# Kernel tuning notes

Hardware: AMD Instinct MI355X
Metric: run time of the kernel (lower is better)

Reference implementation:

```python
import jax, jax.numpy as jnp
import numpy as np

EPS_BN = 1e-5
CLAMP_MAX = 1e-10  # nn.Hardtanh(min_val=0, max_val=1e-10) on squared dists


def _three_nn(xyz1, xyz2):
    # xyz1: (b, n, 3), xyz2: (b, m, 3) -> sq dists (b, n, 3), idx (b, n, 3)
    d2 = (jnp.sum(xyz1 ** 2, -1, keepdims=True)
          - 2.0 * jnp.einsum('bnc,bmc->bnm', xyz1, xyz2)
          + jnp.sum(xyz2 ** 2, -1)[:, None, :])  # (b, n, m)
    neg, idx = jax.lax.top_k(-d2, 3)
    return -neg, idx


def _conv_bn_relu(x, W, b, g, beta):
    # x: (b, n, cin); 1x1 Conv2d == pointwise linear, BN over (batch, spatial)
    y = jnp.einsum('bnc,oc->bno', x, W) + b
    mean = jnp.mean(y, axis=(0, 1))
    var = jnp.mean((y - mean) ** 2, axis=(0, 1))
    y = (y - mean) * jax.lax.rsqrt(var + EPS_BN) * g + beta
    return jax.nn.relu(y)


def setup_inputs() -> dict:
    key = jax.random.key(0)
    ks = jax.random.split(key, 8)
    b, n, m, c1, c2 = 16, 4096, 1024, 256, 512
    mlp, dimin = [256, 256], [c1 + c2, 256]
    inp = {
        'xyz1': jax.random.normal(ks[0], (b, n, 3), jnp.float32),
        'xyz2': jax.random.normal(ks[1], (b, m, 3), jnp.float32),
        'points1': jax.random.normal(ks[2], (b, n, c1), jnp.float32),
        'points2': jax.random.normal(ks[3], (b, m, c2), jnp.float32),
        'W1': jax.random.normal(ks[4], (mlp[0], dimin[0]), jnp.float32) * 0.02,
        'b1': jnp.zeros((mlp[0],), jnp.float32),
        'g1': jnp.ones((mlp[0],), jnp.float32),
        'beta1': jnp.zeros((mlp[0],), jnp.float32),
        'W2': jax.random.normal(ks[5], (mlp[1], dimin[1]), jnp.float32) * 0.02,
        'b2': jnp.zeros((mlp[1],), jnp.float32),
        'g2': jnp.ones((mlp[1],), jnp.float32),
        'beta2': jnp.zeros((mlp[1],), jnp.float32),
    }
    return inp


def reference(xyz1, xyz2, points1, points2, W1, b1, g1, beta1, W2, b2, g2, beta2):
    dist, idx = _three_nn(xyz1, xyz2)                     # (b, n, 3)
    dist = jnp.clip(dist, 0.0, CLAMP_MAX)                 # Hardtanh(0, 1e-10)
    inv = 1.0 / dist
    weight = inv / jnp.sum(inv, axis=2, keepdims=True)    # (b, n, 3)
    neigh = jax.vmap(lambda p, i: p[i])(points2, idx)     # (b, n, 3, c2)
    interp = jnp.einsum('bnk,bnkc->bnc', weight, neigh)   # (b, n, c2)
    feat = jnp.concatenate([interp, points1], axis=2)     # (b, n, c2+c1)
    feat = _conv_bn_relu(feat, W1, b1, g1, beta1)
    feat = _conv_bn_relu(feat, W2, b2, g2, beta2)
    return jnp.transpose(feat, (0, 2, 1))                 # (b, c_out, n)
```

## Files before the change

### kernel.cpp

```cpp
#include <hip/hip_runtime.h>

typedef unsigned short u16;
typedef short sh8 __attribute__((ext_vector_type(8)));
typedef float floatx4 __attribute__((ext_vector_type(4)));
typedef float float4v __attribute__((ext_vector_type(4)));
typedef u16 us8 __attribute__((ext_vector_type(8)));

#define NB    16
#define NPTS  4096
#define MPTS  1024
#define CC1   256
#define CC2   512
#define KK1   768
#define CCO   256
#define MT    (NB*NPTS)
#define MZ    (NB*MPTS)

__device__ __forceinline__ float b2f(u16 u) {
    union { unsigned i; float f; } v; v.i = ((unsigned)u) << 16; return v.f;
}
__device__ __forceinline__ u16 f2b(float f) {
    union { float f; unsigned i; } v; v.f = f;
    unsigned u = v.i;
    unsigned r = (u + 0x7fffu + ((u >> 16) & 1u)) >> 16;
    return (u16)r;
}
__device__ __forceinline__ float ldv(const void* p, size_t i, int f32) {
    return f32 ? ((const float*)p)[i] : b2f(((const u16*)p)[i]);
}
__device__ __forceinline__ void stv(void* p, size_t i, int f32, float v) {
    if (f32) ((float*)p)[i] = v; else ((u16*)p)[i] = f2b(v);
}
__device__ __forceinline__ void gl_lds16(const void* g, void* l) {
    __builtin_amdgcn_global_load_lds(
        (const __attribute__((address_space(1))) void*)g,
        (__attribute__((address_space(3))) void*)l, 16, 0, 0);
}

__global__ void Pointnet_fp_module_33071248179394_kernel(
        const unsigned* g1bits, int* flag, float* stats) {
    int i = blockIdx.x * 256 + threadIdx.x;
    stats[i] = 0.f;
    if (i == 0) flag[0] = (g1bits[0] == 0x3F800000u) ? 1 : 0;
}

__global__ __launch_bounds__(256) void three_nn_k(
        const int* flagp, const void* xyz1, const void* xyz2,
        int* nidx, float* nw) {
    __shared__ float4 P[MPTS];
    __shared__ float md[256][3];
    __shared__ int   mi[256][3];
    const int f32 = flagp[0];
    const int bi = blockIdx.x >> 6;
    const int chunk = blockIdx.x & 63;
    const int t = threadIdx.x;
    const int ql = t & 63, sp = t >> 6;

    for (int p = t; p < MPTS; p += 256) {
        size_t s = (size_t)(bi * MPTS + p) * 3;
        P[p] = make_float4(ldv(xyz2, s, f32), ldv(xyz2, s + 1, f32),
                           ldv(xyz2, s + 2, f32), 0.f);
    }
    __syncthreads();

    const int q = chunk * 64 + ql;
    size_t s1 = (size_t)(bi * NPTS + q) * 3;
    const float qx = ldv(xyz1, s1 + 0, f32);
    const float qy = ldv(xyz1, s1 + 1, f32);
    const float qz = ldv(xyz1, s1 + 2, f32);

    float d0 = 3e38f, d1 = 3e38f, dv2 = 3e38f;
    int i0 = -1, i1 = -1, i2 = -1;
    const int jbeg = sp * 256, jend = jbeg + 256;
    #pragma unroll 4
    for (int j = jbeg; j < jend; j++) {
        float4 p = P[j];
        float dx = qx - p.x;
        float dy = qy - p.y;
        float dz = qz - p.z;
        float dd = fmaf(dx, dx, fmaf(dy, dy, dz * dz));
        if (dd < dv2) {
            if (dd < d0)      { dv2 = d1; i2 = i1; d1 = d0; i1 = i0; d0 = dd; i0 = j; }
            else if (dd < d1) { dv2 = d1; i2 = i1; d1 = dd; i1 = j; }
            else              { dv2 = dd; i2 = j; }
        }
    }
    md[t][0] = d0;  md[t][1] = d1;  md[t][2] = dv2;
    mi[t][0] = i0;  mi[t][1] = i1;  mi[t][2] = i2;
    __syncthreads();

    if (t < 64) {
        float b0 = 3e38f, b1 = 3e38f, b2v = 3e38f;
        int j0 = -1, j1 = -1, j2 = -1;
        #pragma unroll
        for (int s = 0; s < 4; s++) {
            int base = s * 64 + t;
            #pragma unroll
            for (int k = 0; k < 3; k++) {
                float d = md[base][k];
                int ji = mi[base][k];
                if (d < b0)      { b2v = b1; j2 = j1; b1 = b0; j1 = j0; b0 = d; j0 = ji; }
                else if (d < b1) { b2v = b1; j2 = j1; b1 = d; j1 = ji; }
                else if (d < b2v){ b2v = d; j2 = ji; }
            }
        }
        float e0 = fminf(fmaxf(b0, 0.f), 1e-10f);
        float e1 = fminf(fmaxf(b1, 0.f), 1e-10f);
        float e2 = fminf(fmaxf(b2v, 0.f), 1e-10f);
        float v0 = 1.0f / e0, v1 = 1.0f / e1, v2 = 1.0f / e2;
        float s = v0 + v1 + v2;
        const size_t gq = ((size_t)bi * NPTS + chunk * 64 + t) * 3;
        nidx[gq + 0] = j0; nidx[gq + 1] = j1; nidx[gq + 2] = j2;
        nw[gq + 0] = v0 / s; nw[gq + 1] = v1 / s; nw[gq + 2] = v2 / s;
    }
}

__global__ __launch_bounds__(256) void cvt_vec_k(
        const int* flagp, const void* src, u16* dst) {
    const int f32 = flagp[0];
    const size_t i = ((size_t)blockIdx.x * 256 + threadIdx.x) * 8;
    us8 o;
    if (f32) {
        float4v a = *(const float4v*)((const float*)src + i);
        float4v b = *(const float4v*)((const float*)src + i + 4);
        #pragma unroll
        for (int k = 0; k < 4; k++) { o[k] = f2b(a[k]); o[k + 4] = f2b(b[k]); }
    } else {
        o = *(const us8*)((const u16*)src + i);
    }
    *(us8*)(dst + i) = o;
}

__global__ __launch_bounds__(256) void cvt_slice_k(
        const int* flagp, const void* src, u16* dst,
        int stride, int off, int cshift) {
    const int f32 = flagp[0];
    const int i = blockIdx.x * 256 + threadIdx.x;
    const int r = i >> cshift, c = i & ((1 << cshift) - 1);
    dst[i] = f2b(ldv(src, (size_t)r * stride + off + c, f32));
}

template<int K>
__global__ __launch_bounds__(256, 2) void gemm_bt(
        const int* flagp, const u16* __restrict__ A, const u16* __restrict__ B,
        const void* __restrict__ bias, u16* __restrict__ Y) {
    __shared__ u16 As[128 * 32];
    __shared__ u16 Bs[128 * 32];
    const int f32 = flagp[0];
    const int tid = threadIdx.x;
    const int m0 = blockIdx.x * 128;
    const int n0 = blockIdx.y * 128;
    const int wave = tid >> 6, lane = tid & 63;
    const int wm = wave & 1, wn = wave >> 1;
    const int l16 = lane & 15, quad = lane >> 4;

    floatx4 acc[4][4];
    #pragma unroll
    for (int i = 0; i < 4; i++)
        #pragma unroll
        for (int j = 0; j < 4; j++)
            acc[i][j] = (floatx4){0.f, 0.f, 0.f, 0.f};

    for (int kb = 0; kb < K; kb += 32) {
        __syncthreads();
        #pragma unroll
        for (int tt = 0; tt < 2; tt++) {
            int chunk = tid + tt * 256;
            int row = chunk >> 2, c4 = chunk & 3;
            gl_lds16(A + (size_t)(m0 + row) * K + kb + c4 * 8, As + chunk * 8);
            gl_lds16(B + (size_t)(n0 + row) * K + kb + c4 * 8, Bs + chunk * 8);
        }
        __syncthreads();

        sh8 af[4], bfr[4];
        #pragma unroll
        for (int i = 0; i < 4; i++)
            af[i] = *(const sh8*)(As + (wm * 64 + i * 16 + l16) * 32 + quad * 8);
        #pragma unroll
        for (int j = 0; j < 4; j++)
            bfr[j] = *(const sh8*)(Bs + (wn * 64 + j * 16 + l16) * 32 + quad * 8);
        #pragma unroll
        for (int i = 0; i < 4; i++)
            #pragma unroll
            for (int j = 0; j < 4; j++)
                acc[i][j] = __builtin_amdgcn_mfma_f32_16x16x32_bf16(
                                af[i], bfr[j], acc[i][j], 0, 0, 0);
    }

    #pragma unroll
    for (int i = 0; i < 4; i++) {
        #pragma unroll
        for (int j = 0; j < 4; j++) {
            int col = n0 + wn * 64 + j * 16 + l16;
            float bv = ldv(bias, col, f32);
            #pragma unroll
            for (int r = 0; r < 4; r++) {
                int row = m0 + wm * 64 + i * 16 + quad * 4 + r;
                Y[(size_t)row * CCO + col] = f2b(acc[i][j][r] + bv);
            }
        }
    }
}

__global__ __launch_bounds__(256, 2) void gemm_p_k(
        const int* flagp, const u16* __restrict__ A, const u16* __restrict__ B,
        const void* __restrict__ bias, const int* __restrict__ nidx,
        const float* __restrict__ nw, const u16* __restrict__ Z,
        u16* __restrict__ Y) {
    __shared__ u16 As[128 * 32];
    __shared__ u16 Bs[128 * 32];
    __shared__ int   sIdx[128 * 3];
    __shared__ float sW[128 * 3];
    const int f32 = flagp[0];
    const int tid = threadIdx.x;
    const int m0 = blockIdx.x * 128;
    const int n0 = blockIdx.y * 128;
    const int wave = tid >> 6, lane = tid & 63;
    const int wm = wave & 1, wn = wave >> 1;
    const int l16 = lane & 15, quad = lane >> 4;
    const int zbase = (m0 >> 12) << 10;

    if (tid < 128) {
        size_t q3 = (size_t)(m0 + tid) * 3;
        #pragma unroll
        for (int k = 0; k < 3; k++) {
            sIdx[tid * 3 + k] = nidx[q3 + k];
            sW[tid * 3 + k]   = nw[q3 + k];
        }
    }

    floatx4 acc[4][4];
    #pragma unroll
    for (int i = 0; i < 4; i++)
        #pragma unroll
        for (int j = 0; j < 4; j++)
            acc[i][j] = (floatx4){0.f, 0.f, 0.f, 0.f};

    constexpr int K = 256;
    for (int kb = 0; kb < K; kb += 32) {
        __syncthreads();
        #pragma unroll
        for (int tt = 0; tt < 2; tt++) {
            int chunk = tid + tt * 256;
            int row = chunk >> 2, c4 = chunk & 3;
            gl_lds16(A + (size_t)(m0 + row) * K + kb + c4 * 8, As + chunk * 8);
            gl_lds16(B + (size_t)(n0 + row) * K + kb + c4 * 8, Bs + chunk * 8);
        }
        __syncthreads();

        sh8 af[4], bfr[4];
        #pragma unroll
        for (int i = 0; i < 4; i++)
            af[i] = *(const sh8*)(As + (wm * 64 + i * 16 + l16) * 32 + quad * 8);
        #pragma unroll
        for (int j = 0; j < 4; j++)
            bfr[j] = *(const sh8*)(Bs + (wn * 64 + j * 16 + l16) * 32 + quad * 8);
        #pragma unroll
        for (int i = 0; i < 4; i++)
            #pragma unroll
            for (int j = 0; j < 4; j++)
                acc[i][j] = __builtin_amdgcn_mfma_f32_16x16x32_bf16(
                                af[i], bfr[j], acc[i][j], 0, 0, 0);
    }

    #pragma unroll
    for (int i = 0; i < 4; i++) {
        #pragma unroll
        for (int r = 0; r < 4; r++) {
            int rl = wm * 64 + i * 16 + quad * 4 + r;
            int i0 = sIdx[rl * 3 + 0], i1 = sIdx[rl * 3 + 1], i2 = sIdx[rl * 3 + 2];
            float w0 = sW[rl * 3 + 0], w1 = sW[rl * 3 + 1], w2 = sW[rl * 3 + 2];
            const u16* z0 = Z + (size_t)(zbase + i0) * CCO;
            const u16* z1 = Z + (size_t)(zbase + i1) * CCO;
            const u16* z2 = Z + (size_t)(zbase + i2) * CCO;
            #pragma unroll
            for (int j = 0; j < 4; j++) {
                int col = n0 + wn * 64 + j * 16 + l16;
                float v = acc[i][j][r] + ldv(bias, col, f32)
                        + w0 * b2f(z0[col]) + w1 * b2f(z1[col]) + w2 * b2f(z2[col]);
                Y[(size_t)(m0 + rl) * CCO + col] = f2b(v);
            }
        }
    }
}

__global__ void bn_stats_k(const u16* Y, float* sum, float* sq) {
    const int c = threadIdx.x;
    const int r0 = blockIdx.x * 128;
    float s = 0.f, ss = 0.f;
    for (int r = 0; r < 128; r++) {
        float v = b2f(Y[(size_t)(r0 + r) * CCO + c]);
        s += v; ss += v * v;
    }
    atomicAdd(&sum[c], s);
    atomicAdd(&sq[c], ss);
}

__global__ void bn_apply_k(const int* flagp, u16* Y,
                           const float* sum, const float* sq,
                           const void* g, const void* beta) {
    const int f32 = flagp[0];
    const int idx = blockIdx.x * 256 + threadIdx.x;
    const int c = idx & (CCO - 1);
    const float invM = 1.0f / (float)MT;
    float mean = sum[c] * invM;
    float var = sq[c] * invM - mean * mean;
    float sc = rsqrtf(var + 1e-5f) * ldv(g, c, f32);
    float sh = ldv(beta, c, f32) - mean * sc;
    float v = b2f(Y[idx]) * sc + sh;
    Y[idx] = f2b(fmaxf(v, 0.f));
}

__global__ void bn_out_k(const int* flagp, const u16* Y, void* Out,
                         const float* sum, const float* sq,
                         const void* g, const void* beta) {
    __shared__ float tile[64][65];
    const int f32 = flagp[0];
    const int bi = blockIdx.z;
    const int p0 = blockIdx.x * 64;
    const int c0 = blockIdx.y * 64;
    const int t = threadIdx.x;
    const int cr = t & 63, rq = t >> 6;
    const float invM = 1.0f / (float)MT;

    const int c = c0 + cr;
    float mean = sum[c] * invM;
    float var = sq[c] * invM - mean * mean;
    float sc = rsqrtf(var + 1e-5f) * ldv(g, c, f32);
    float sh = ldv(beta, c, f32) - mean * sc;

    for (int r = rq; r < 64; r += 4) {
        int m = bi * NPTS + p0 + r;
        float v = b2f(Y[(size_t)m * CCO + c]) * sc + sh;
        tile[r][cr] = fmaxf(v, 0.f);
    }
    __syncthreads();
    for (int r = rq; r < 64; r += 4) {
        size_t o = ((size_t)bi * CCO + (c0 + r)) * NPTS + p0 + cr;
        stv(Out, o, f32, tile[cr][r]);
    }
}

extern "C" void kernel_launch(void* const* d_in, const int* in_sizes, int n_in,
                              void* d_out, int out_size, void* d_ws, size_t ws_size,
                              hipStream_t stream) {
    const void* xyz1    = d_in[0];
    const void* xyz2    = d_in[1];
    const void* points1 = d_in[2];
    const void* points2 = d_in[3];
    const void* W1      = d_in[4];
    const void* b1      = d_in[5];
    const void* g1      = d_in[6];
    const void* be1     = d_in[7];
    const void* W2      = d_in[8];
    const void* b2      = d_in[9];
    const void* g2      = d_in[10];
    const void* be2     = d_in[11];
    char* ws = (char*)d_ws;

    int*   flag  = (int*)(ws + 0);
    float* sum1  = (float*)(ws + 4096);
    float* sq1   = (float*)(ws + 5120);
    float* sum2  = (float*)(ws + 6144);
    float* sq2   = (float*)(ws + 7168);
    float* zeros = (float*)(ws + 8192);
    int*   nidx  = (int*)(ws + 20480);
    float* nw    = (float*)(ws + 806912);
    u16* Wa   = (u16*)(ws + 2097152);
    u16* Wbp  = (u16*)(ws + 2359296);
    u16* W2b  = (u16*)(ws + 2490368);
    u16* Z    = (u16*)(ws + 2621440);
    u16* p2b  = (u16*)(ws + 11010048ULL);
    u16* p1b  = (u16*)(ws + 27787264ULL);
    u16* y1   = (u16*)(ws + 61341696ULL);
    u16* y2   = (u16*)(ws + 94896128ULL);

    Pointnet_fp_module_33071248179394_kernel<<<dim3(16), dim3(256), 0, stream>>>(
        (const unsigned*)g1, flag, (float*)(ws + 4096));
    cvt_slice_k<<<dim3(CCO * CC2 / 256), dim3(256), 0, stream>>>(flag, W1, Wa, KK1, 0, 9);
    cvt_slice_k<<<dim3(CCO * CC1 / 256), dim3(256), 0, stream>>>(flag, W1, Wbp, KK1, CC2, 8);
    cvt_slice_k<<<dim3(CCO * CCO / 256), dim3(256), 0, stream>>>(flag, W2, W2b, CCO, 0, 8);
    cvt_vec_k<<<dim3(MZ * CC2 / 2048), dim3(256), 0, stream>>>(flag, points2, p2b);
    cvt_vec_k<<<dim3(MT * CC1 / 2048), dim3(256), 0, stream>>>(flag, points1, p1b);
    three_nn_k<<<dim3(1024), dim3(256), 0, stream>>>(flag, xyz1, xyz2, nidx, nw);
    gemm_bt<CC2><<<dim3(MZ / 128, CCO / 128), dim3(256), 0, stream>>>(flag, p2b, Wa, zeros, Z);
    gemm_p_k<<<dim3(MT / 128, CCO / 128), dim3(256), 0, stream>>>(
        flag, p1b, Wbp, b1, nidx, nw, Z, y1);
    bn_stats_k<<<dim3(512), dim3(256), 0, stream>>>(y1, sum1, sq1);
    bn_apply_k<<<dim3(MT), dim3(256), 0, stream>>>(flag, y1, sum1, sq1, g1, be1);
    gemm_bt<CCO><<<dim3(MT / 128, CCO / 128), dim3(256), 0, stream>>>(flag, y1, W2b, b2, y2);
    bn_stats_k<<<dim3(512), dim3(256), 0, stream>>>(y2, sum2, sq2);
    bn_out_k<<<dim3(64, 4, NB), dim3(256), 0, stream>>>(flag, y2, d_out, sum2, sq2, g2, be2);
}
```

Baseline: 359.3 us.

## Fuse BN statistics into GEMM epilogues and merge conversion kernels

```diff
diff --git a/kernel.cpp b/kernel.cpp
--- a/kernel.cpp
+++ b/kernel.cpp
@@ -44,19 +44,19 @@
     if (i == 0) flag[0] = (g1bits[0] == 0x3F800000u) ? 1 : 0;
 }
 
-__global__ __launch_bounds__(256) void three_nn_k(
+__global__ __launch_bounds__(512) void three_nn_k(
         const int* flagp, const void* xyz1, const void* xyz2,
         int* nidx, float* nw) {
     __shared__ float4 P[MPTS];
-    __shared__ float md[256][3];
-    __shared__ int   mi[256][3];
+    __shared__ float md[512][3];
+    __shared__ int   mi[512][3];
     const int f32 = flagp[0];
     const int bi = blockIdx.x >> 6;
     const int chunk = blockIdx.x & 63;
     const int t = threadIdx.x;
     const int ql = t & 63, sp = t >> 6;
 
-    for (int p = t; p < MPTS; p += 256) {
+    for (int p = t; p < MPTS; p += 512) {
         size_t s = (size_t)(bi * MPTS + p) * 3;
         P[p] = make_float4(ldv(xyz2, s, f32), ldv(xyz2, s + 1, f32),
                            ldv(xyz2, s + 2, f32), 0.f);
@@ -71,7 +71,7 @@
 
     float d0 = 3e38f, d1 = 3e38f, dv2 = 3e38f;
     int i0 = -1, i1 = -1, i2 = -1;
-    const int jbeg = sp * 256, jend = jbeg + 256;
+    const int jbeg = sp * 128, jend = jbeg + 128;
     #pragma unroll 4
     for (int j = jbeg; j < jend; j++) {
         float4 p = P[j];
@@ -93,7 +93,7 @@
         float b0 = 3e38f, b1 = 3e38f, b2v = 3e38f;
         int j0 = -1, j1 = -1, j2 = -1;
         #pragma unroll
-        for (int s = 0; s < 4; s++) {
+        for (int s = 0; s < 8; s++) {
             int base = s * 64 + t;
             #pragma unroll
             for (int k = 0; k < 3; k++) {
@@ -115,37 +115,53 @@
     }
 }
 
-__global__ __launch_bounds__(256) void cvt_vec_k(
-        const int* flagp, const void* src, u16* dst) {
-    const int f32 = flagp[0];
-    const size_t i = ((size_t)blockIdx.x * 256 + threadIdx.x) * 8;
+__global__ __launch_bounds__(256) void cvt_w_k(
+        const int* flagp, const void* W1, const void* W2,
+        u16* Wa, u16* Wbp, u16* W2b) {
+    const int f32 = flagp[0];
+    const int i = blockIdx.x * 256 + threadIdx.x;
+    if (i < CCO * CC2) {
+        int r = i >> 9, c = i & 511;
+        Wa[i] = f2b(ldv(W1, (size_t)r * KK1 + c, f32));
+    } else if (i < CCO * CC2 + CCO * CC1) {
+        int k = i - CCO * CC2;
+        int r = k >> 8, c = k & 255;
+        Wbp[k] = f2b(ldv(W1, (size_t)r * KK1 + CC2 + c, f32));
+    } else {
+        int k = i - CCO * CC2 - CCO * CC1;
+        W2b[k] = f2b(ldv(W2, k, f32));
+    }
+}
+
+__global__ __launch_bounds__(256) void cvt_pts_k(
+        const int* flagp, const void* p2, const void* p1,
+        u16* p2b, u16* p1b) {
+    const int f32 = flagp[0];
+    size_t i = ((size_t)blockIdx.x * 256 + threadIdx.x) * 8;
+    const size_t N2 = (size_t)MZ * CC2;
+    const void* src; u16* dst; size_t off;
+    if (i < N2) { src = p2; dst = p2b; off = i; }
+    else        { src = p1; dst = p1b; off = i - N2; }
     us8 o;
     if (f32) {
-        float4v a = *(const float4v*)((const float*)src + i);
-        float4v b = *(const float4v*)((const float*)src + i + 4);
+        float4v a = *(const float4v*)((const float*)src + off);
+        float4v b = *(const float4v*)((const float*)src + off + 4);
         #pragma unroll
         for (int k = 0; k < 4; k++) { o[k] = f2b(a[k]); o[k + 4] = f2b(b[k]); }
     } else {
-        o = *(const us8*)((const u16*)src + i);
-    }
-    *(us8*)(dst + i) = o;
-}
-
-__global__ __launch_bounds__(256) void cvt_slice_k(
-        const int* flagp, const void* src, u16* dst,
-        int stride, int off, int cshift) {
-    const int f32 = flagp[0];
-    const int i = blockIdx.x * 256 + threadIdx.x;
-    const int r = i >> cshift, c = i & ((1 << cshift) - 1);
-    dst[i] = f2b(ldv(src, (size_t)r * stride + off + c, f32));
-}
-
-template<int K>
+        o = *(const us8*)((const u16*)src + off);
+    }
+    *(us8*)(dst + off) = o;
+}
+
+template<int K, bool STATS>
 __global__ __launch_bounds__(256, 2) void gemm_bt(
         const int* flagp, const u16* __restrict__ A, const u16* __restrict__ B,
-        const void* __restrict__ bias, u16* __restrict__ Y) {
+        const void* __restrict__ bias, u16* __restrict__ Y,
+        float* __restrict__ sum, float* __restrict__ sq) {
     __shared__ u16 As[128 * 32];
     __shared__ u16 Bs[128 * 32];
+    __shared__ float sSum[128], sSq[128];
     const int f32 = flagp[0];
     const int tid = threadIdx.x;
     const int m0 = blockIdx.x * 128;
@@ -154,6 +170,8 @@
     const int wm = wave & 1, wn = wave >> 1;
     const int l16 = lane & 15, quad = lane >> 4;
 
+    if (STATS && tid < 128) { sSum[tid] = 0.f; sSq[tid] = 0.f; }
+
     floatx4 acc[4][4];
     #pragma unroll
     for (int i = 0; i < 4; i++)
@@ -187,6 +205,7 @@
                                 af[i], bfr[j], acc[i][j], 0, 0, 0);
     }
 
+    float cs[4] = {0.f, 0.f, 0.f, 0.f}, css[4] = {0.f, 0.f, 0.f, 0.f};
     #pragma unroll
     for (int i = 0; i < 4; i++) {
         #pragma unroll
@@ -196,8 +215,23 @@
             #pragma unroll
             for (int r = 0; r < 4; r++) {
                 int row = m0 + wm * 64 + i * 16 + quad * 4 + r;
-                Y[(size_t)row * CCO + col] = f2b(acc[i][j][r] + bv);
+                float v = acc[i][j][r] + bv;
+                if (STATS) { cs[j] += v; css[j] += v * v; }
+                Y[(size_t)row * CCO + col] = f2b(v);
             }
+        }
+    }
+    if (STATS) {
+        #pragma unroll
+        for (int j = 0; j < 4; j++) {
+            int cl = wn * 64 + j * 16 + l16;
+            atomicAdd(&sSum[cl], cs[j]);
+            atomicAdd(&sSq[cl], css[j]);
+        }
+        __syncthreads();
+        if (tid < 128) {
+            atomicAdd(&sum[n0 + tid], sSum[tid]);
+            atomicAdd(&sq[n0 + tid], sSq[tid]);
         }
     }
 }
@@ -206,11 +240,12 @@
         const int* flagp, const u16* __restrict__ A, const u16* __restrict__ B,
         const void* __restrict__ bias, const int* __restrict__ nidx,
         const float* __restrict__ nw, const u16* __restrict__ Z,
-        u16* __restrict__ Y) {
+        u16* __restrict__ Y, float* __restrict__ sum, float* __restrict__ sq) {
     __shared__ u16 As[128 * 32];
     __shared__ u16 Bs[128 * 32];
     __shared__ int   sIdx[128 * 3];
     __shared__ float sW[128 * 3];
+    __shared__ float sSum[128], sSq[128];
     const int f32 = flagp[0];
     const int tid = threadIdx.x;
     const int m0 = blockIdx.x * 128;
@@ -227,6 +262,7 @@
             sIdx[tid * 3 + k] = nidx[q3 + k];
             sW[tid * 3 + k]   = nw[q3 + k];
         }
+        sSum[tid] = 0.f; sSq[tid] = 0.f;
     }
 
     floatx4 acc[4][4];
@@ -263,6 +299,7 @@
                                 af[i], bfr[j], acc[i][j], 0, 0, 0);
     }
 
+    float cs[4] = {0.f, 0.f, 0.f, 0.f}, css[4] = {0.f, 0.f, 0.f, 0.f};
     #pragma unroll
     for (int i = 0; i < 4; i++) {
         #pragma unroll
@@ -278,37 +315,51 @@
                 int col = n0 + wn * 64 + j * 16 + l16;
                 float v = acc[i][j][r] + ldv(bias, col, f32)
                         + w0 * b2f(z0[col]) + w1 * b2f(z1[col]) + w2 * b2f(z2[col]);
+                cs[j] += v; css[j] += v * v;
                 Y[(size_t)(m0 + rl) * CCO + col] = f2b(v);
             }
         }
     }
-}
-
-__global__ void bn_stats_k(const u16* Y, float* sum, float* sq) {
-    const int c = threadIdx.x;
-    const int r0 = blockIdx.x * 128;
-    float s = 0.f, ss = 0.f;
-    for (int r = 0; r < 128; r++) {
-        float v = b2f(Y[(size_t)(r0 + r) * CCO + c]);
-        s += v; ss += v * v;
-    }
-    atomicAdd(&sum[c], s);
-    atomicAdd(&sq[c], ss);
-}
-
-__global__ void bn_apply_k(const int* flagp, u16* Y,
-                           const float* sum, const float* sq,
-                           const void* g, const void* beta) {
-    const int f32 = flagp[0];
-    const int idx = blockIdx.x * 256 + threadIdx.x;
-    const int c = idx & (CCO - 1);
-    const float invM = 1.0f / (float)MT;
-    float mean = sum[c] * invM;
-    float var = sq[c] * invM - mean * mean;
-    float sc = rsqrtf(var + 1e-5f) * ldv(g, c, f32);
-    float sh = ldv(beta, c, f32) - mean * sc;
-    float v = b2f(Y[idx]) * sc + sh;
-    Y[idx] = f2b(fmaxf(v, 0.f));
+    #pragma unroll
+    for (int j = 0; j < 4; j++) {
+        int cl = wn * 64 + j * 16 + l16;
+        atomicAdd(&sSum[cl], cs[j]);
+        atomicAdd(&sSq[cl], css[j]);
+    }
+    __syncthreads();
+    if (tid < 128) {
+        atomicAdd(&sum[n0 + tid], sSum[tid]);
+        atomicAdd(&sq[n0 + tid], sSq[tid]);
+    }
+}
+
+__global__ __launch_bounds__(256) void bn_apply_k(
+        const int* flagp, u16* Y, const float* sum, const float* sq,
+        const void* g, const void* beta) {
+    __shared__ float ssc[CCO], ssh[CCO];
+    const int f32 = flagp[0];
+    const int t = threadIdx.x;
+    {
+        const float invM = 1.0f / (float)MT;
+        float mean = sum[t] * invM;
+        float var = sq[t] * invM - mean * mean;
+        float sc = rsqrtf(var + 1e-5f) * ldv(g, t, f32);
+        ssc[t] = sc;
+        ssh[t] = ldv(beta, t, f32) - mean * sc;
+    }
+    __syncthreads();
+    const size_t base = ((size_t)blockIdx.x * 256 + t) * 16;
+    const int c0 = (int)(base & (CCO - 1));
+    us8 a = *(const us8*)(Y + base);
+    us8 b = *(const us8*)(Y + base + 8);
+    us8 oa, ob;
+    #pragma unroll
+    for (int k = 0; k < 8; k++) {
+        oa[k] = f2b(fmaxf(b2f((u16)a[k]) * ssc[c0 + k] + ssh[c0 + k], 0.f));
+        ob[k] = f2b(fmaxf(b2f((u16)b[k]) * ssc[c0 + 8 + k] + ssh[c0 + 8 + k], 0.f));
+    }
+    *(us8*)(Y + base) = oa;
+    *(us8*)(Y + base + 8) = ob;
 }
 
 __global__ void bn_out_k(const int* flagp, const u16* Y, void* Out,
@@ -377,18 +428,19 @@
 
     Pointnet_fp_module_33071248179394_kernel<<<dim3(16), dim3(256), 0, stream>>>(
         (const unsigned*)g1, flag, (float*)(ws + 4096));
-    cvt_slice_k<<<dim3(CCO * CC2 / 256), dim3(256), 0, stream>>>(flag, W1, Wa, KK1, 0, 9);
-    cvt_slice_k<<<dim3(CCO * CC1 / 256), dim3(256), 0, stream>>>(flag, W1, Wbp, KK1, CC2, 8);
-    cvt_slice_k<<<dim3(CCO * CCO / 256), dim3(256), 0, stream>>>(flag, W2, W2b, CCO, 0, 8);
-    cvt_vec_k<<<dim3(MZ * CC2 / 2048), dim3(256), 0, stream>>>(flag, points2, p2b);
-    cvt_vec_k<<<dim3(MT * CC1 / 2048), dim3(256), 0, stream>>>(flag, points1, p1b);
-    three_nn_k<<<dim3(1024), dim3(256), 0, stream>>>(flag, xyz1, xyz2, nidx, nw);
-    gemm_bt<CC2><<<dim3(MZ / 128, CCO / 128), dim3(256), 0, stream>>>(flag, p2b, Wa, zeros, Z);
+    cvt_w_k<<<dim3(1024), dim3(256), 0, stream>>>(
+        flag, W1, W2, Wa, Wbp, W2b);
+    cvt_pts_k<<<dim3((MZ * CC2 + MT * CC1) / 2048), dim3(256), 0, stream>>>(
+        flag, points2, points1, p2b, p1b);
+    three_nn_k<<<dim3(1024), dim3(512), 0, stream>>>(flag, xyz1, xyz2, nidx, nw);
+    gemm_bt<CC2, false><<<dim3(MZ / 128, CCO / 128), dim3(256), 0, stream>>>(
+        flag, p2b, Wa, zeros, Z, nullptr, nullptr);
     gemm_p_k<<<dim3(MT / 128, CCO / 128), dim3(256), 0, stream>>>(
-        flag, p1b, Wbp, b1, nidx, nw, Z, y1);
-    bn_stats_k<<<dim3(512), dim3(256), 0, stream>>>(y1, sum1, sq1);
-    bn_apply_k<<<dim3(MT), dim3(256), 0, stream>>>(flag, y1, sum1, sq1, g1, be1);
-    gemm_bt<CCO><<<dim3(MT / 128, CCO / 128), dim3(256), 0, stream>>>(flag, y1, W2b, b2, y2);
-    bn_stats_k<<<dim3(512), dim3(256), 0, stream>>>(y2, sum2, sq2);
-    bn_out_k<<<dim3(64, 4, NB), dim3(256), 0, stream>>>(flag, y2, d_out, sum2, sq2, g2, be2);
-}
+        flag, p1b, Wbp, b1, nidx, nw, Z, y1, sum1, sq1);
+    bn_apply_k<<<dim3(MT * CCO / 4096), dim3(256), 0, stream>>>(
+        flag, y1, sum1, sq1, g1, be1);
+    gemm_bt<CCO, true><<<dim3(MT / 128, CCO / 128), dim3(256), 0, stream>>>(
+        flag, y1, W2b, b2, y2, sum2, sq2);
+    bn_out_k<<<dim3(64, 4, NB), dim3(256), 0, stream>>>(
+        flag, y2, d_out, sum2, sq2, g2, be2);
+}
```

Result: faster. 337.8 us (-6.0%).
